# Performance work log

Measured on AMD Instinct MI355X. Metric: run time of the kernel, lower is better.

Reference implementation:

```python
import jax, jax.numpy as jnp
import numpy as np

B, N, DK = 16, 2048, 512

def setup_inputs() -> dict:
    key = jax.random.key(0)
    k1, k2, k3, k4 = jax.random.split(key, 4)
    return {
        'src_embedding': jax.random.normal(k1, (B, N, DK), dtype=jnp.float32),
        'target_embedding': jax.random.normal(k2, (B, N, DK), dtype=jnp.float32),
        'src': jax.random.normal(k3, (B, N, 3), dtype=jnp.float32),
        'target': jax.random.normal(k4, (B, N, 3), dtype=jnp.float32),
    }

def reference(src_embedding, target_embedding, src, target):
    d_k = src_embedding.shape[2]
    # attention-weighted soft correspondence: [B, N, M]
    scores = jnp.einsum('bnd,bmd->bnm', src_embedding, target_embedding)
    scores = jax.nn.softmax(scores / jnp.sqrt(jnp.asarray(d_k, scores.dtype)), axis=2)
    tgt_corr = jnp.einsum('bnm,bmc->bnc', scores, src)            # [B, N, 3]
    tgt_mean = jnp.mean(target, axis=1, keepdims=True)            # [B, 1, 3]
    corr_mean = jnp.mean(tgt_corr, axis=1, keepdims=True)         # [B, 1, 3]
    # cross-covariance H = (target - mu_t)^T @ (tgt_corr - mu_c): [B, 3, 3]
    H = jnp.einsum('bnc,bnd->bcd', target - tgt_mean, tgt_corr - corr_mean)
    U, S, Vh = jnp.linalg.svd(H)                                  # H = U diag(S) Vh
    det = jnp.linalg.det(jnp.matmul(U, Vh))                       # [B]
    # C = diag(1, 1, det) reflection fix; R = U @ C @ Vh
    diag = jnp.stack([jnp.ones_like(det), jnp.ones_like(det), det], axis=-1)  # [B, 3]
    R = jnp.matmul(U * diag[:, None, :], Vh)                      # [B, 3, 3]
    # t^T = mu_t^T - R @ mu_c^T, returned as [B, 1, 3]
    t = tgt_mean - jnp.einsum('bij,bkj->bki', R, corr_mean)
    return (R, t)
```

## Files before the change

kernel.cpp:

```cpp
#include <hip/hip_runtime.h>
#include <hip/hip_bf16.h>
#include <stdint.h>


#define B_  16
#define N_  2048
#define DK_ 512
#define SCALE 0.044194173824159216f

typedef __bf16 bf16x8 __attribute__((ext_vector_type(8)));
typedef float  f32x16 __attribute__((ext_vector_type(16)));
typedef float  f32x4  __attribute__((ext_vector_type(4)));

union BF8 { bf16x8 v; unsigned u[4]; };

__device__ inline unsigned pkbf(float a, float b) {
  unsigned r;
  asm("v_cvt_pk_bf16_f32 %0, %1, %2" : "=v"(r) : "v"(a), "v"(b));
  return r;
}

__global__ __launch_bounds__(512, 2)
void attn_stats_kernel(const float* __restrict__ Q, const float* __restrict__ K,
                       const float* __restrict__ Vsrc, float* __restrict__ part)
{
  __shared__ __align__(16) unsigned char s_k[32 * 1024];
  __shared__ __align__(16) float s_srcT[3 * 1024];

  const int L   = blockIdx.x;
  const int xcd = L & 7;
  const int kk  = L >> 3;
  const int b   = xcd + 8 * (kk & 1);
  const int ms  = (kk >> 1) & 1;
  const int nb  = kk >> 2;

  const int tid  = threadIdx.x;
  const int lane = tid & 63;
  const int wid  = tid >> 6;
  const int row  = lane & 31;
  const int hi   = lane >> 5;

  const int mchunk0 = ms * 1024;

  {
    const float* vp = Vsrc + ((size_t)b * N_ + mchunk0) * 3;
    for (int idx = tid; idx < 3072; idx += 512) {
      int m = idx / 3, c = idx - 3 * m;
      s_srcT[c * 1024 + m] = vp[idx];
    }
  }

  const int qglob = nb * 256 + wid * 32 + row;
  BF8 qf[32];
  {
    const f32x4* qp = (const f32x4*)(Q + ((size_t)b * N_ + qglob) * DK_);
    #pragma unroll
    for (int t = 0; t < 32; ++t) {
      f32x4 f0 = qp[t * 4 + hi * 2];
      f32x4 f1 = qp[t * 4 + hi * 2 + 1];
      qf[t].u[0] = pkbf(f0[0], f0[1]);
      qf[t].u[1] = pkbf(f0[2], f0[3]);
      qf[t].u[2] = pkbf(f1[0], f1[1]);
      qf[t].u[3] = pkbf(f1[2], f1[3]);
    }
  }

  const f32x4* kg = (const f32x4*)(K + ((size_t)b * N_ + mchunk0) * DK_);

  float lsum = 0.f, a0 = 0.f, a1 = 0.f, a2 = 0.f;

  f32x4 stg[8];
  #pragma unroll
  for (int i = 0; i < 8; ++i) stg[i] = kg[i * 512 + tid];

  const unsigned kread_base = (unsigned)(row * 1024);
  const unsigned kread_xor  = (unsigned)(row << 4);

  for (int tile = 0; tile < 32; ++tile) {
    __syncthreads();
    #pragma unroll
    for (int i = 0; i < 8; ++i) {
      int idx  = i * 512 + tid;
      int r    = idx >> 7;
      int colb = (idx & 127) * 8;
      unsigned addr = (unsigned)(r * 1024) + ((unsigned)colb ^ ((unsigned)(r << 4)));
      uint2 w2;
      w2.x = pkbf(stg[i][0], stg[i][1]);
      w2.y = pkbf(stg[i][2], stg[i][3]);
      *(uint2*)(s_k + addr) = w2;
    }
    __syncthreads();
    if (tile + 1 < 32) {
      const f32x4* kt = kg + (size_t)(tile + 1) * 4096;
      #pragma unroll
      for (int i = 0; i < 8; ++i) stg[i] = kt[i * 512 + tid];
    }
    f32x16 sc0, sc1;
    #pragma unroll
    for (int i = 0; i < 16; ++i) { sc0[i] = 0.f; sc1[i] = 0.f; }
    #pragma unroll
    for (int t = 0; t < 32; t += 2) {
      BF8 kf0, kf1;
      kf0.v = *(const bf16x8*)(s_k + kread_base +
                (((unsigned)(t * 32 + hi * 16)) ^ kread_xor));
      sc0 = __builtin_amdgcn_mfma_f32_32x32x16_bf16(kf0.v, qf[t].v, sc0, 0, 0, 0);
      kf1.v = *(const bf16x8*)(s_k + kread_base +
                (((unsigned)((t + 1) * 32 + hi * 16)) ^ kread_xor));
      sc1 = __builtin_amdgcn_mfma_f32_32x32x16_bf16(kf1.v, qf[t + 1].v, sc1, 0, 0, 0);
    }
    #pragma unroll
    for (int j = 0; j < 4; ++j) {
      const int mrun = tile * 32 + j * 8 + hi * 4;
      f32x4 s0 = *(const f32x4*)&s_srcT[mrun];
      f32x4 s1 = *(const f32x4*)&s_srcT[1024 + mrun];
      f32x4 s2 = *(const f32x4*)&s_srcT[2048 + mrun];
      #pragma unroll
      for (int i2 = 0; i2 < 4; ++i2) {
        float w = __expf((sc0[j * 4 + i2] + sc1[j * 4 + i2]) * SCALE);
        lsum += w;
        a0 += w * s0[i2];
        a1 += w * s1[i2];
        a2 += w * s2[i2];
      }
    }
  }

  a0   += __shfl_xor(a0, 32);
  a1   += __shfl_xor(a1, 32);
  a2   += __shfl_xor(a2, 32);
  lsum += __shfl_xor(lsum, 32);

  if (hi == 0) {
    f32x4 o; o[0] = a0; o[1] = a1; o[2] = a2; o[3] = lsum;
    *(f32x4*)(part + (((size_t)ms * B_ + b) * N_ + qglob) * 4) = o;
  }
}

__global__ void reduce_kernel(const float* __restrict__ part,
                              const float* __restrict__ tgt,
                              float* __restrict__ ws2)
{
  const int b = blockIdx.x, tid = threadIdx.x;
  float s[15];
  #pragma unroll
  for (int j = 0; j < 15; ++j) s[j] = 0.f;

  for (int n = tid; n < N_; n += 256) {
    f32x4 p0 = *(const f32x4*)(part + (((size_t)0 * B_ + b) * N_ + n) * 4);
    f32x4 p1 = *(const f32x4*)(part + (((size_t)1 * B_ + b) * N_ + n) * 4);
    float inv = 1.0f / (p0[3] + p1[3]);
    float c0 = (p0[0] + p1[0]) * inv;
    float c1 = (p0[1] + p1[1]) * inv;
    float c2 = (p0[2] + p1[2]) * inv;
    const float* tp = tgt + ((size_t)b * N_ + n) * 3;
    float t0 = tp[0], t1 = tp[1], t2 = tp[2];
    s[0] += t0;  s[1] += t1;  s[2] += t2;
    s[3] += c0;  s[4] += c1;  s[5] += c2;
    s[6] += t0 * c0;  s[7]  += t0 * c1;  s[8]  += t0 * c2;
    s[9] += t1 * c0;  s[10] += t1 * c1;  s[11] += t1 * c2;
    s[12] += t2 * c0; s[13] += t2 * c1;  s[14] += t2 * c2;
  }
  #pragma unroll
  for (int j = 0; j < 15; ++j) {
    #pragma unroll
    for (int off = 32; off > 0; off >>= 1) s[j] += __shfl_xor(s[j], off);
  }
  __shared__ float red[4][15];
  int lane = tid & 63, w = tid >> 6;
  if (lane == 0) {
    #pragma unroll
    for (int j = 0; j < 15; ++j) red[w][j] = s[j];
  }
  __syncthreads();
  if (tid < 15)
    ws2[b * 16 + tid] = red[0][tid] + red[1][tid] + red[2][tid] + red[3][tid];
}

__device__ inline void jrot(double A[3][3], double V[3][3], int p, int q) {
  double apq = A[p][q];
  if (fabs(apq) < 1e-300) return;
  double tau = (A[q][q] - A[p][p]) / (2.0 * apq);
  double tt = (tau >= 0.0) ? 1.0 / (tau + sqrt(1.0 + tau * tau))
                           : 1.0 / (tau - sqrt(1.0 + tau * tau));
  double c = 1.0 / sqrt(1.0 + tt * tt), sn = tt * c;
  for (int k = 0; k < 3; ++k) {
    double akp = A[k][p], akq = A[k][q];
    A[k][p] = c * akp - sn * akq;
    A[k][q] = sn * akp + c * akq;
  }
  for (int k = 0; k < 3; ++k) {
    double apk = A[p][k], aqk = A[q][k];
    A[p][k] = c * apk - sn * aqk;
    A[q][k] = sn * apk + c * aqk;
  }
  for (int k = 0; k < 3; ++k) {
    double vkp = V[k][p], vkq = V[k][q];
    V[k][p] = c * vkp - sn * vkq;
    V[k][q] = sn * vkp + c * vkq;
  }
}

__global__ void svd_kernel(const float* __restrict__ ws2, float* __restrict__ out)
{
  const int b = threadIdx.x;
  if (b >= B_) return;
  const float* s = ws2 + b * 16;
  const double invN = 1.0 / (double)N_;
  double stv[3] = {s[0], s[1], s[2]};
  double scv[3] = {s[3], s[4], s[5]};
  double H[3][3];
  for (int c = 0; c < 3; ++c)
    for (int d = 0; d < 3; ++d)
      H[c][d] = (double)s[6 + c * 3 + d] - stv[c] * scv[d] * invN;

  double A[3][3], V[3][3] = {{1,0,0},{0,1,0},{0,0,1}};
  for (int i = 0; i < 3; ++i)
    for (int j = 0; j < 3; ++j) {
      double acc = 0.0;
      for (int c = 0; c < 3; ++c) acc += H[c][i] * H[c][j];
      A[i][j] = acc;
    }
  for (int sw = 0; sw < 15; ++sw) { jrot(A,V,0,1); jrot(A,V,0,2); jrot(A,V,1,2); }

  double e[3] = {A[0][0], A[1][1], A[2][2]};
  double vc[3][3];
  for (int k = 0; k < 3; ++k)
    for (int i = 0; i < 3; ++i) vc[k][i] = V[i][k];
  for (int a2 = 0; a2 < 2; ++a2)
    for (int b2 = 0; b2 < 2 - a2; ++b2)
      if (e[b2] < e[b2 + 1]) {
        double te = e[b2]; e[b2] = e[b2 + 1]; e[b2 + 1] = te;
        for (int i = 0; i < 3; ++i) {
          double tv = vc[b2][i]; vc[b2][i] = vc[b2 + 1][i]; vc[b2 + 1][i] = tv;
        }
      }

  double u1[3], u2[3], u3[3];
  for (int i = 0; i < 3; ++i)
    u1[i] = H[i][0]*vc[0][0] + H[i][1]*vc[0][1] + H[i][2]*vc[0][2];
  double n1 = sqrt(u1[0]*u1[0] + u1[1]*u1[1] + u1[2]*u1[2]);
  n1 = fmax(n1, 1e-300);
  for (int i = 0; i < 3; ++i) u1[i] /= n1;
  for (int i = 0; i < 3; ++i)
    u2[i] = H[i][0]*vc[1][0] + H[i][1]*vc[1][1] + H[i][2]*vc[1][2];
  double d12 = u1[0]*u2[0] + u1[1]*u2[1] + u1[2]*u2[2];
  for (int i = 0; i < 3; ++i) u2[i] -= d12 * u1[i];
  double n2 = sqrt(u2[0]*u2[0] + u2[1]*u2[1] + u2[2]*u2[2]);
  n2 = fmax(n2, 1e-300);
  for (int i = 0; i < 3; ++i) u2[i] /= n2;
  u3[0] = u1[1]*u2[2] - u1[2]*u2[1];
  u3[1] = u1[2]*u2[0] - u1[0]*u2[2];
  u3[2] = u1[0]*u2[1] - u1[1]*u2[0];

  double detV = vc[0][0]*(vc[1][1]*vc[2][2] - vc[1][2]*vc[2][1])
              - vc[0][1]*(vc[1][0]*vc[2][2] - vc[1][2]*vc[2][0])
              + vc[0][2]*(vc[1][0]*vc[2][1] - vc[1][1]*vc[2][0]);

  double R[3][3];
  for (int i = 0; i < 3; ++i)
    for (int j = 0; j < 3; ++j)
      R[i][j] = u1[i]*vc[0][j] + u2[i]*vc[1][j] + detV * u3[i]*vc[2][j];

  for (int i = 0; i < 3; ++i)
    for (int j = 0; j < 3; ++j)
      out[b * 9 + i * 3 + j] = (float)R[i][j];

  double muc[3] = {scv[0]*invN, scv[1]*invN, scv[2]*invN};
  for (int i = 0; i < 3; ++i) {
    double ti = stv[i]*invN - (R[i][0]*muc[0] + R[i][1]*muc[1] + R[i][2]*muc[2]);
    out[B_ * 9 + b * 3 + i] = (float)ti;
  }
}

extern "C" void kernel_launch(void* const* d_in, const int* in_sizes, int n_in,
                              void* d_out, int out_size, void* d_ws, size_t ws_size,
                              hipStream_t stream)
{
  const float* srcE = (const float*)d_in[0];
  const float* tgtE = (const float*)d_in[1];
  const float* srcP = (const float*)d_in[2];
  const float* tgtP = (const float*)d_in[3];
  float* out  = (float*)d_out;
  float* part = (float*)d_ws;
  float* ws2  = part + (size_t)2 * B_ * N_ * 4;

  attn_stats_kernel<<<dim3(256), dim3(512), 0, stream>>>(srcE, tgtE, srcP, part);
  reduce_kernel<<<dim3(B_), dim3(256), 0, stream>>>(part, tgtP, ws2);
  svd_kernel<<<dim3(1), dim3(64), 0, stream>>>(ws2, out);
}
```

Measured before the change: 143.5 us.

## Double-buffer K tiles in LDS with smaller blocks and half-K stages

Measured after the change: 357.5 us. 2.49x slower.

```diff
diff --git a/kernel.cpp b/kernel.cpp
--- a/kernel.cpp
+++ b/kernel.cpp
@@ -20,19 +20,20 @@
   return r;
 }
 
-__global__ __launch_bounds__(512, 2)
+__global__ __launch_bounds__(256, 2)
 void attn_stats_kernel(const float* __restrict__ Q, const float* __restrict__ K,
                        const float* __restrict__ Vsrc, float* __restrict__ part)
 {
-  __shared__ __align__(16) unsigned char s_k[32 * 1024];
+  __shared__ __align__(16) unsigned char s_k[2][32 * 256 * 2];
   __shared__ __align__(16) float s_srcT[3 * 1024];
 
   const int L   = blockIdx.x;
   const int xcd = L & 7;
-  const int kk  = L >> 3;
-  const int b   = xcd + 8 * (kk & 1);
-  const int ms  = (kk >> 1) & 1;
-  const int nb  = kk >> 2;
+  const int k   = L >> 3;
+  const int b   = xcd + 8 * (k & 1);
+  const int rem = k >> 1;
+  const int nb  = rem & 15;
+  const int ms  = rem >> 4;
 
   const int tid  = threadIdx.x;
   const int lane = tid & 63;
@@ -44,13 +45,13 @@
 
   {
     const float* vp = Vsrc + ((size_t)b * N_ + mchunk0) * 3;
-    for (int idx = tid; idx < 3072; idx += 512) {
+    for (int idx = tid; idx < 3072; idx += 256) {
       int m = idx / 3, c = idx - 3 * m;
       s_srcT[c * 1024 + m] = vp[idx];
     }
   }
 
-  const int qglob = nb * 256 + wid * 32 + row;
+  const int qglob = nb * 128 + wid * 32 + row;
   BF8 qf[32];
   {
     const f32x4* qp = (const f32x4*)(Q + ((size_t)b * N_ + qglob) * DK_);
@@ -67,62 +68,90 @@
 
   const f32x4* kg = (const f32x4*)(K + ((size_t)b * N_ + mchunk0) * DK_);
 
+  #define STG_LOAD(u)                                                        \
+    {                                                                        \
+      const int mt_ = (u) >> 1, h_ = (u) & 1;                                \
+      _Pragma("unroll")                                                      \
+      for (int i = 0; i < 8; ++i) {                                          \
+        int idx = i * 256 + tid;                                             \
+        int r_  = idx >> 6, c4 = idx & 63;                                   \
+        stg[i] = kg[(size_t)(mt_ * 32 + r_) * 128 + h_ * 64 + c4];           \
+      }                                                                      \
+    }
+
+  #define STG_WRITE(bb)                                                      \
+    {                                                                        \
+      _Pragma("unroll")                                                      \
+      for (int i = 0; i < 8; ++i) {                                          \
+        int idx = i * 256 + tid;                                             \
+        int r_  = idx >> 6;                                                  \
+        unsigned colb = (unsigned)((idx & 63) * 8);                          \
+        unsigned addr = (unsigned)(r_ * 512) + (colb ^ ((unsigned)((r_ & 7) << 4))); \
+        uint2 w2;                                                            \
+        w2.x = pkbf(stg[i][0], stg[i][1]);                                   \
+        w2.y = pkbf(stg[i][2], stg[i][3]);                                   \
+        *(uint2*)(&s_k[bb][0] + addr) = w2;                                  \
+      }                                                                      \
+    }
+
+  f32x4 stg[8];
   float lsum = 0.f, a0 = 0.f, a1 = 0.f, a2 = 0.f;
 
-  f32x4 stg[8];
+  f32x16 sc0, sc1;
   #pragma unroll
-  for (int i = 0; i < 8; ++i) stg[i] = kg[i * 512 + tid];
-
-  const unsigned kread_base = (unsigned)(row * 1024);
-  const unsigned kread_xor  = (unsigned)(row << 4);
-
-  for (int tile = 0; tile < 32; ++tile) {
+  for (int i = 0; i < 16; ++i) { sc0[i] = 0.f; sc1[i] = 0.f; }
+
+  STG_LOAD(0)
+  STG_WRITE(0)
+  STG_LOAD(1)
+  __syncthreads();
+
+  const unsigned kread_base = (unsigned)(row * 512);
+  const unsigned kread_xor  = (unsigned)((row & 7) << 4);
+
+  const int NT = 64;
+  for (int t = 0; t < NT; ++t) {
+    const int cur = t & 1;
+    if (t + 1 < NT) STG_WRITE(cur ^ 1)
+    if (t + 2 < NT) STG_LOAD(t + 2)
+
+    const int h = t & 1;
+    const unsigned char* bp = &s_k[cur][0];
+    __builtin_amdgcn_s_setprio(1);
+    #pragma unroll
+    for (int ks = 0; ks < 16; ks += 2) {
+      BF8 kf0, kf1;
+      kf0.v = *(const bf16x8*)(bp + kread_base +
+                (((unsigned)(ks * 32 + hi * 16)) ^ kread_xor));
+      sc0 = __builtin_amdgcn_mfma_f32_32x32x16_bf16(kf0.v, qf[h * 16 + ks].v, sc0, 0, 0, 0);
+      kf1.v = *(const bf16x8*)(bp + kread_base +
+                (((unsigned)((ks + 1) * 32 + hi * 16)) ^ kread_xor));
+      sc1 = __builtin_amdgcn_mfma_f32_32x32x16_bf16(kf1.v, qf[h * 16 + ks + 1].v, sc1, 0, 0, 0);
+    }
+    __builtin_amdgcn_s_setprio(0);
+
+    if (t & 1) {
+      const int mt = t >> 1;
+      #pragma unroll
+      for (int j = 0; j < 4; ++j) {
+        const int mrun = mt * 32 + j * 8 + hi * 4;
+        f32x4 s0 = *(const f32x4*)&s_srcT[mrun];
+        f32x4 s1 = *(const f32x4*)&s_srcT[1024 + mrun];
+        f32x4 s2 = *(const f32x4*)&s_srcT[2048 + mrun];
+        #pragma unroll
+        for (int i2 = 0; i2 < 4; ++i2) {
+          float w = __expf((sc0[j * 4 + i2] + sc1[j * 4 + i2]) * SCALE);
+          lsum += w;
+          a0 += w * s0[i2];
+          a1 += w * s1[i2];
+          a2 += w * s2[i2];
+        }
+      }
+      #pragma unroll
+      for (int i = 0; i < 16; ++i) { sc0[i] = 0.f; sc1[i] = 0.f; }
+    }
+
     __syncthreads();
-    #pragma unroll
-    for (int i = 0; i < 8; ++i) {
-      int idx  = i * 512 + tid;
-      int r    = idx >> 7;
-      int colb = (idx & 127) * 8;
-      unsigned addr = (unsigned)(r * 1024) + ((unsigned)colb ^ ((unsigned)(r << 4)));
-      uint2 w2;
-      w2.x = pkbf(stg[i][0], stg[i][1]);
-      w2.y = pkbf(stg[i][2], stg[i][3]);
-      *(uint2*)(s_k + addr) = w2;
-    }
-    __syncthreads();
-    if (tile + 1 < 32) {
-      const f32x4* kt = kg + (size_t)(tile + 1) * 4096;
-      #pragma unroll
-      for (int i = 0; i < 8; ++i) stg[i] = kt[i * 512 + tid];
-    }
-    f32x16 sc0, sc1;
-    #pragma unroll
-    for (int i = 0; i < 16; ++i) { sc0[i] = 0.f; sc1[i] = 0.f; }
-    #pragma unroll
-    for (int t = 0; t < 32; t += 2) {
-      BF8 kf0, kf1;
-      kf0.v = *(const bf16x8*)(s_k + kread_base +
-                (((unsigned)(t * 32 + hi * 16)) ^ kread_xor));
-      sc0 = __builtin_amdgcn_mfma_f32_32x32x16_bf16(kf0.v, qf[t].v, sc0, 0, 0, 0);
-      kf1.v = *(const bf16x8*)(s_k + kread_base +
-                (((unsigned)((t + 1) * 32 + hi * 16)) ^ kread_xor));
-      sc1 = __builtin_amdgcn_mfma_f32_32x32x16_bf16(kf1.v, qf[t + 1].v, sc1, 0, 0, 0);
-    }
-    #pragma unroll
-    for (int j = 0; j < 4; ++j) {
-      const int mrun = tile * 32 + j * 8 + hi * 4;
-      f32x4 s0 = *(const f32x4*)&s_srcT[mrun];
-      f32x4 s1 = *(const f32x4*)&s_srcT[1024 + mrun];
-      f32x4 s2 = *(const f32x4*)&s_srcT[2048 + mrun];
-      #pragma unroll
-      for (int i2 = 0; i2 < 4; ++i2) {
-        float w = __expf((sc0[j * 4 + i2] + sc1[j * 4 + i2]) * SCALE);
-        lsum += w;
-        a0 += w * s0[i2];
-        a1 += w * s1[i2];
-        a2 += w * s2[i2];
-      }
-    }
   }
 
   a0   += __shfl_xor(a0, 32);
@@ -134,6 +163,8 @@
     f32x4 o; o[0] = a0; o[1] = a1; o[2] = a2; o[3] = lsum;
     *(f32x4*)(part + (((size_t)ms * B_ + b) * N_ + qglob) * 4) = o;
   }
+  #undef STG_LOAD
+  #undef STG_WRITE
 }
 
 __global__ void reduce_kernel(const float* __restrict__ part,
@@ -284,7 +315,7 @@
   float* part = (float*)d_ws;
   float* ws2  = part + (size_t)2 * B_ * N_ * 4;
 
-  attn_stats_kernel<<<dim3(256), dim3(512), 0, stream>>>(srcE, tgtE, srcP, part);
+  attn_stats_kernel<<<dim3(512), dim3(256), 0, stream>>>(srcE, tgtE, srcP, part);
   reduce_kernel<<<dim3(B_), dim3(256), 0, stream>>>(part, tgtP, ws2);
   svd_kernel<<<dim3(1), dim3(64), 0, stream>>>(ws2, out);
 }
```

## Remap attention blocks so each processes two batches over strided key windows

Applied to the files above, without the earlier changes.

Result: slower. 175.5 us (+22.3%).

```diff
diff --git a/kernel.cpp b/kernel.cpp
--- a/kernel.cpp
+++ b/kernel.cpp
@@ -25,14 +25,13 @@
                        const float* __restrict__ Vsrc, float* __restrict__ part)
 {
   __shared__ __align__(16) unsigned char s_k[32 * 1024];
-  __shared__ __align__(16) float s_srcT[3 * 1024];
+  __shared__ __align__(16) float s_srcT[3 * 256];
 
   const int L   = blockIdx.x;
-  const int xcd = L & 7;
-  const int kk  = L >> 3;
-  const int b   = xcd + 8 * (kk & 1);
-  const int ms  = (kk >> 1) & 1;
-  const int nb  = kk >> 2;
+  const int x   = L & 7;
+  const int cu  = L >> 3;
+  const int nb  = cu & 7;
+  const int sms = cu >> 3;
 
   const int tid  = threadIdx.x;
   const int lane = tid & 63;
@@ -40,99 +39,110 @@
   const int row  = lane & 31;
   const int hi   = lane >> 5;
 
-  const int mchunk0 = ms * 1024;
-
-  {
-    const float* vp = Vsrc + ((size_t)b * N_ + mchunk0) * 3;
-    for (int idx = tid; idx < 3072; idx += 512) {
-      int m = idx / 3, c = idx - 3 * m;
-      s_srcT[c * 1024 + m] = vp[idx];
-    }
-  }
-
   const int qglob = nb * 256 + wid * 32 + row;
-  BF8 qf[32];
-  {
-    const f32x4* qp = (const f32x4*)(Q + ((size_t)b * N_ + qglob) * DK_);
-    #pragma unroll
-    for (int t = 0; t < 32; ++t) {
-      f32x4 f0 = qp[t * 4 + hi * 2];
-      f32x4 f1 = qp[t * 4 + hi * 2 + 1];
-      qf[t].u[0] = pkbf(f0[0], f0[1]);
-      qf[t].u[1] = pkbf(f0[2], f0[3]);
-      qf[t].u[2] = pkbf(f1[0], f1[1]);
-      qf[t].u[3] = pkbf(f1[2], f1[3]);
-    }
-  }
-
-  const f32x4* kg = (const f32x4*)(K + ((size_t)b * N_ + mchunk0) * DK_);
-
-  float lsum = 0.f, a0 = 0.f, a1 = 0.f, a2 = 0.f;
-
-  f32x4 stg[8];
-  #pragma unroll
-  for (int i = 0; i < 8; ++i) stg[i] = kg[i * 512 + tid];
 
   const unsigned kread_base = (unsigned)(row * 1024);
   const unsigned kread_xor  = (unsigned)(row << 4);
 
-  for (int tile = 0; tile < 32; ++tile) {
-    __syncthreads();
-    #pragma unroll
-    for (int i = 0; i < 8; ++i) {
-      int idx  = i * 512 + tid;
-      int r    = idx >> 7;
-      int colb = (idx & 127) * 8;
-      unsigned addr = (unsigned)(r * 1024) + ((unsigned)colb ^ ((unsigned)(r << 4)));
-      uint2 w2;
-      w2.x = pkbf(stg[i][0], stg[i][1]);
-      w2.y = pkbf(stg[i][2], stg[i][3]);
-      *(uint2*)(s_k + addr) = w2;
-    }
-    __syncthreads();
-    if (tile + 1 < 32) {
-      const f32x4* kt = kg + (size_t)(tile + 1) * 4096;
+  BF8   qf[32];
+  f32x4 stg[8];
+
+  for (int half = 0; half < 2; ++half) {
+    const int b = x + 8 * half;
+
+    {
+      const f32x4* qp = (const f32x4*)(Q + ((size_t)b * N_ + qglob) * DK_);
       #pragma unroll
-      for (int i = 0; i < 8; ++i) stg[i] = kt[i * 512 + tid];
-    }
-    f32x16 sc0, sc1;
-    #pragma unroll
-    for (int i = 0; i < 16; ++i) { sc0[i] = 0.f; sc1[i] = 0.f; }
-    #pragma unroll
-    for (int t = 0; t < 32; t += 2) {
-      BF8 kf0, kf1;
-      kf0.v = *(const bf16x8*)(s_k + kread_base +
-                (((unsigned)(t * 32 + hi * 16)) ^ kread_xor));
-      sc0 = __builtin_amdgcn_mfma_f32_32x32x16_bf16(kf0.v, qf[t].v, sc0, 0, 0, 0);
-      kf1.v = *(const bf16x8*)(s_k + kread_base +
-                (((unsigned)((t + 1) * 32 + hi * 16)) ^ kread_xor));
-      sc1 = __builtin_amdgcn_mfma_f32_32x32x16_bf16(kf1.v, qf[t + 1].v, sc1, 0, 0, 0);
-    }
-    #pragma unroll
-    for (int j = 0; j < 4; ++j) {
-      const int mrun = tile * 32 + j * 8 + hi * 4;
-      f32x4 s0 = *(const f32x4*)&s_srcT[mrun];
-      f32x4 s1 = *(const f32x4*)&s_srcT[1024 + mrun];
-      f32x4 s2 = *(const f32x4*)&s_srcT[2048 + mrun];
-      #pragma unroll
-      for (int i2 = 0; i2 < 4; ++i2) {
-        float w = __expf((sc0[j * 4 + i2] + sc1[j * 4 + i2]) * SCALE);
-        lsum += w;
-        a0 += w * s0[i2];
-        a1 += w * s1[i2];
-        a2 += w * s2[i2];
+      for (int t = 0; t < 32; ++t) {
+        f32x4 f0 = qp[t * 4 + hi * 2];
+        f32x4 f1 = qp[t * 4 + hi * 2 + 1];
+        qf[t].u[0] = pkbf(f0[0], f0[1]);
+        qf[t].u[1] = pkbf(f0[2], f0[3]);
+        qf[t].u[2] = pkbf(f1[0], f1[1]);
+        qf[t].u[3] = pkbf(f1[2], f1[3]);
       }
     }
-  }
-
-  a0   += __shfl_xor(a0, 32);
-  a1   += __shfl_xor(a1, 32);
-  a2   += __shfl_xor(a2, 32);
-  lsum += __shfl_xor(lsum, 32);
-
-  if (hi == 0) {
-    f32x4 o; o[0] = a0; o[1] = a1; o[2] = a2; o[3] = lsum;
-    *(f32x4*)(part + (((size_t)ms * B_ + b) * N_ + qglob) * 4) = o;
+
+    float lsum = 0.f, a0 = 0.f, a1 = 0.f, a2 = 0.f;
+
+    for (int ph = 0; ph < 2; ++ph) {
+      const int mwin = ph * 1024 + sms * 256;
+      const f32x4* kg = (const f32x4*)(K + ((size_t)b * N_ + mwin) * DK_);
+
+      __syncthreads();
+
+      {
+        const float* vp = Vsrc + ((size_t)b * N_ + mwin) * 3;
+        for (int idx = tid; idx < 768; idx += 512) {
+          int m = idx / 3, c = idx - 3 * m;
+          s_srcT[c * 256 + m] = vp[idx];
+        }
+      }
+
+      #pragma unroll
+      for (int i = 0; i < 8; ++i) stg[i] = kg[i * 512 + tid];
+
+      for (int t = 0; t < 8; ++t) {
+        __syncthreads();
+        #pragma unroll
+        for (int i = 0; i < 8; ++i) {
+          int idx  = i * 512 + tid;
+          int r    = idx >> 7;
+          int colb = (idx & 127) * 8;
+          unsigned addr = (unsigned)(r * 1024) + ((unsigned)colb ^ ((unsigned)(r << 4)));
+          uint2 w2;
+          w2.x = pkbf(stg[i][0], stg[i][1]);
+          w2.y = pkbf(stg[i][2], stg[i][3]);
+          *(uint2*)(s_k + addr) = w2;
+        }
+        __syncthreads();
+        if (t + 1 < 8) {
+          const f32x4* kt = kg + (size_t)(t + 1) * 4096;
+          #pragma unroll
+          for (int i = 0; i < 8; ++i) stg[i] = kt[i * 512 + tid];
+        }
+        f32x16 sc0, sc1;
+        #pragma unroll
+        for (int i = 0; i < 16; ++i) { sc0[i] = 0.f; sc1[i] = 0.f; }
+        __builtin_amdgcn_s_setprio(1);
+        #pragma unroll
+        for (int ks = 0; ks < 32; ks += 2) {
+          BF8 kf0, kf1;
+          kf0.v = *(const bf16x8*)(s_k + kread_base +
+                    (((unsigned)(ks * 32 + hi * 16)) ^ kread_xor));
+          sc0 = __builtin_amdgcn_mfma_f32_32x32x16_bf16(kf0.v, qf[ks].v, sc0, 0, 0, 0);
+          kf1.v = *(const bf16x8*)(s_k + kread_base +
+                    (((unsigned)((ks + 1) * 32 + hi * 16)) ^ kread_xor));
+          sc1 = __builtin_amdgcn_mfma_f32_32x32x16_bf16(kf1.v, qf[ks + 1].v, sc1, 0, 0, 0);
+        }
+        __builtin_amdgcn_s_setprio(0);
+        #pragma unroll
+        for (int j = 0; j < 4; ++j) {
+          const int mrun = t * 32 + j * 8 + hi * 4;
+          f32x4 s0 = *(const f32x4*)&s_srcT[mrun];
+          f32x4 s1 = *(const f32x4*)&s_srcT[256 + mrun];
+          f32x4 s2 = *(const f32x4*)&s_srcT[512 + mrun];
+          #pragma unroll
+          for (int i2 = 0; i2 < 4; ++i2) {
+            float w = __expf((sc0[j * 4 + i2] + sc1[j * 4 + i2]) * SCALE);
+            lsum += w;
+            a0 += w * s0[i2];
+            a1 += w * s1[i2];
+            a2 += w * s2[i2];
+          }
+        }
+      }
+    }
+
+    a0   += __shfl_xor(a0, 32);
+    a1   += __shfl_xor(a1, 32);
+    a2   += __shfl_xor(a2, 32);
+    lsum += __shfl_xor(lsum, 32);
+
+    if (hi == 0) {
+      f32x4 o; o[0] = a0; o[1] = a1; o[2] = a2; o[3] = lsum;
+      *(f32x4*)(part + (((size_t)sms * B_ + b) * N_ + qglob) * 4) = o;
+    }
   }
 }
 
@@ -148,10 +158,13 @@
   for (int n = tid; n < N_; n += 256) {
     f32x4 p0 = *(const f32x4*)(part + (((size_t)0 * B_ + b) * N_ + n) * 4);
     f32x4 p1 = *(const f32x4*)(part + (((size_t)1 * B_ + b) * N_ + n) * 4);
-    float inv = 1.0f / (p0[3] + p1[3]);
-    float c0 = (p0[0] + p1[0]) * inv;
-    float c1 = (p0[1] + p1[1]) * inv;
-    float c2 = (p0[2] + p1[2]) * inv;
+    f32x4 p2 = *(const f32x4*)(part + (((size_t)2 * B_ + b) * N_ + n) * 4);
+    f32x4 p3 = *(const f32x4*)(part + (((size_t)3 * B_ + b) * N_ + n) * 4);
+    float l  = p0[3] + p1[3] + p2[3] + p3[3];
+    float inv = 1.0f / l;
+    float c0 = (p0[0] + p1[0] + p2[0] + p3[0]) * inv;
+    float c1 = (p0[1] + p1[1] + p2[1] + p3[1]) * inv;
+    float c2 = (p0[2] + p1[2] + p2[2] + p3[2]) * inv;
     const float* tp = tgt + ((size_t)b * N_ + n) * 3;
     float t0 = tp[0], t1 = tp[1], t2 = tp[2];
     s[0] += t0;  s[1] += t1;  s[2] += t2;
@@ -282,7 +295,7 @@
   const float* tgtP = (const float*)d_in[3];
   float* out  = (float*)d_out;
   float* part = (float*)d_ws;
-  float* ws2  = part + (size_t)2 * B_ * N_ * 4;
+  float* ws2  = part + (size_t)4 * B_ * N_ * 4;
 
   attn_stats_kernel<<<dim3(256), dim3(512), 0, stream>>>(srcE, tgtE, srcP, part);
   reduce_kernel<<<dim3(B_), dim3(256), 0, stream>>>(part, tgtP, ws2);
```

## Pre-convert K to bf16 and stream tiles into double-buffered LDS via direct loads

Applied to the files above, without the earlier changes.

New measurement: 131.8 us. 1.09x faster.

```diff
diff --git a/kernel.cpp b/kernel.cpp
--- a/kernel.cpp
+++ b/kernel.cpp
@@ -20,9 +20,149 @@
   return r;
 }
 
+__device__ inline void gl_lds16(const void* g, void* l) {
+  __builtin_amdgcn_global_load_lds(
+      (const __attribute__((address_space(1))) unsigned int*)g,
+      (__attribute__((address_space(3))) unsigned int*)l, 16, 0, 0);
+}
+
+__global__ __launch_bounds__(256)
+void cvt_k_kernel(const float* __restrict__ in, uint4* __restrict__ out)
+{
+  const size_t total = (size_t)B_ * N_ * DK_ / 8;
+  for (size_t i = (size_t)blockIdx.x * 256 + threadIdx.x; i < total;
+       i += (size_t)gridDim.x * 256) {
+    f32x4 a = ((const f32x4*)in)[2 * i];
+    f32x4 c = ((const f32x4*)in)[2 * i + 1];
+    uint4 w;
+    w.x = pkbf(a[0], a[1]);
+    w.y = pkbf(a[2], a[3]);
+    w.z = pkbf(c[0], c[1]);
+    w.w = pkbf(c[2], c[3]);
+    out[i] = w;
+  }
+}
+
 __global__ __launch_bounds__(512, 2)
-void attn_stats_kernel(const float* __restrict__ Q, const float* __restrict__ K,
+void attn_stats_kernel(const float* __restrict__ Q,
+                       const unsigned char* __restrict__ Kbf,
                        const float* __restrict__ Vsrc, float* __restrict__ part)
+{
+  __shared__ __align__(16) unsigned char s_k[2][32 * 1024];
+  __shared__ __align__(16) float s_srcT[3 * 1024];
+
+  const int L   = blockIdx.x;
+  const int xcd = L & 7;
+  const int kk  = L >> 3;
+  const int b   = xcd + 8 * (kk & 1);
+  const int ms  = (kk >> 1) & 1;
+  const int nb  = kk >> 2;
+
+  const int tid  = threadIdx.x;
+  const int lane = tid & 63;
+  const int wid  = tid >> 6;
+  const int row  = lane & 31;
+  const int hi   = lane >> 5;
+
+  const int mchunk0 = ms * 1024;
+
+  {
+    const float* vp = Vsrc + ((size_t)b * N_ + mchunk0) * 3;
+    for (int idx = tid; idx < 3072; idx += 512) {
+      int m = idx / 3, c = idx - 3 * m;
+      s_srcT[c * 1024 + m] = vp[idx];
+    }
+  }
+
+  const int qglob = nb * 256 + wid * 32 + row;
+  BF8 qf[32];
+  {
+    const f32x4* qp = (const f32x4*)(Q + ((size_t)b * N_ + qglob) * DK_);
+    #pragma unroll
+    for (int t = 0; t < 32; ++t) {
+      f32x4 f0 = qp[t * 4 + hi * 2];
+      f32x4 f1 = qp[t * 4 + hi * 2 + 1];
+      qf[t].u[0] = pkbf(f0[0], f0[1]);
+      qf[t].u[1] = pkbf(f0[2], f0[3]);
+      qf[t].u[2] = pkbf(f1[0], f1[1]);
+      qf[t].u[3] = pkbf(f1[2], f1[3]);
+    }
+  }
+
+  const unsigned char* kbase = Kbf + ((size_t)b * N_ + mchunk0) * (DK_ * 2);
+
+  #define STAGE(bb, t)                                                       \
+    { _Pragma("unroll")                                                      \
+      for (int j = 0; j < 4; ++j) {                                          \
+        const int r_ = wid * 4 + j;                                          \
+        gl_lds16(kbase + (((size_t)(t) * 32 + r_) << 10)                     \
+                       + (unsigned)((lane ^ r_) << 4),                       \
+                 &s_k[bb][r_ << 10]);                                        \
+      } }
+
+  float lsum = 0.f, a0 = 0.f, a1 = 0.f, a2 = 0.f;
+
+  const unsigned kread_base = (unsigned)(row * 1024);
+  const unsigned kread_xor  = (unsigned)(row << 4);
+
+  STAGE(0, 0)
+  __syncthreads();
+
+  for (int tile = 0; tile < 32; ++tile) {
+    const int cur = tile & 1;
+    if (tile + 1 < 32) STAGE(cur ^ 1, tile + 1)
+
+    const unsigned char* bp = &s_k[cur][0];
+    f32x16 sc0, sc1;
+    #pragma unroll
+    for (int i = 0; i < 16; ++i) { sc0[i] = 0.f; sc1[i] = 0.f; }
+    __builtin_amdgcn_s_setprio(1);
+    #pragma unroll
+    for (int t = 0; t < 32; t += 2) {
+      BF8 kf0, kf1;
+      kf0.v = *(const bf16x8*)(bp + kread_base +
+                (((unsigned)(t * 32 + hi * 16)) ^ kread_xor));
+      sc0 = __builtin_amdgcn_mfma_f32_32x32x16_bf16(kf0.v, qf[t].v, sc0, 0, 0, 0);
+      kf1.v = *(const bf16x8*)(bp + kread_base +
+                (((unsigned)((t + 1) * 32 + hi * 16)) ^ kread_xor));
+      sc1 = __builtin_amdgcn_mfma_f32_32x32x16_bf16(kf1.v, qf[t + 1].v, sc1, 0, 0, 0);
+    }
+    __builtin_amdgcn_s_setprio(0);
+
+    #pragma unroll
+    for (int j = 0; j < 4; ++j) {
+      const int mrun = tile * 32 + j * 8 + hi * 4;
+      f32x4 s0 = *(const f32x4*)&s_srcT[mrun];
+      f32x4 s1 = *(const f32x4*)&s_srcT[1024 + mrun];
+      f32x4 s2 = *(const f32x4*)&s_srcT[2048 + mrun];
+      #pragma unroll
+      for (int i2 = 0; i2 < 4; ++i2) {
+        float w = __expf((sc0[j * 4 + i2] + sc1[j * 4 + i2]) * SCALE);
+        lsum += w;
+        a0 += w * s0[i2];
+        a1 += w * s1[i2];
+        a2 += w * s2[i2];
+      }
+    }
+
+    __syncthreads();
+  }
+  #undef STAGE
+
+  a0   += __shfl_xor(a0, 32);
+  a1   += __shfl_xor(a1, 32);
+  a2   += __shfl_xor(a2, 32);
+  lsum += __shfl_xor(lsum, 32);
+
+  if (hi == 0) {
+    f32x4 o; o[0] = a0; o[1] = a1; o[2] = a2; o[3] = lsum;
+    *(f32x4*)(part + (((size_t)ms * B_ + b) * N_ + qglob) * 4) = o;
+  }
+}
+
+__global__ __launch_bounds__(512, 2)
+void attn_stats_f32_kernel(const float* __restrict__ Q, const float* __restrict__ K,
+                           const float* __restrict__ Vsrc, float* __restrict__ part)
 {
   __shared__ __align__(16) unsigned char s_k[32 * 1024];
   __shared__ __align__(16) float s_srcT[3 * 1024];
@@ -98,6 +238,7 @@
     f32x16 sc0, sc1;
     #pragma unroll
     for (int i = 0; i < 16; ++i) { sc0[i] = 0.f; sc1[i] = 0.f; }
+    __builtin_amdgcn_s_setprio(1);
     #pragma unroll
     for (int t = 0; t < 32; t += 2) {
       BF8 kf0, kf1;
@@ -108,6 +249,7 @@
                 (((unsigned)((t + 1) * 32 + hi * 16)) ^ kread_xor));
       sc1 = __builtin_amdgcn_mfma_f32_32x32x16_bf16(kf1.v, qf[t + 1].v, sc1, 0, 0, 0);
     }
+    __builtin_amdgcn_s_setprio(0);
     #pragma unroll
     for (int j = 0; j < 4; ++j) {
       const int mrun = tile * 32 + j * 8 + hi * 4;
@@ -280,11 +422,24 @@
   const float* tgtE = (const float*)d_in[1];
   const float* srcP = (const float*)d_in[2];
   const float* tgtP = (const float*)d_in[3];
-  float* out  = (float*)d_out;
-  float* part = (float*)d_ws;
-  float* ws2  = part + (size_t)2 * B_ * N_ * 4;
-
-  attn_stats_kernel<<<dim3(256), dim3(512), 0, stream>>>(srcE, tgtE, srcP, part);
-  reduce_kernel<<<dim3(B_), dim3(256), 0, stream>>>(part, tgtP, ws2);
-  svd_kernel<<<dim3(1), dim3(64), 0, stream>>>(ws2, out);
-}
+  float* out = (float*)d_out;
+
+  const size_t kbf_bytes   = (size_t)B_ * N_ * DK_ * 2;
+  const size_t part_floats = (size_t)2 * B_ * N_ * 4;
+
+  if (ws_size >= kbf_bytes + part_floats * 4 + 1024) {
+    unsigned char* kbf = (unsigned char*)d_ws;
+    float* part = (float*)(kbf + kbf_bytes);
+    float* ws2  = part + part_floats;
+    cvt_k_kernel<<<dim3(2048), dim3(256), 0, stream>>>(tgtE, (uint4*)kbf);
+    attn_stats_kernel<<<dim3(256), dim3(512), 0, stream>>>(srcE, kbf, srcP, part);
+    reduce_kernel<<<dim3(B_), dim3(256), 0, stream>>>(part, tgtP, ws2);
+    svd_kernel<<<dim3(1), dim3(64), 0, stream>>>(ws2, out);
+  } else {
+    float* part = (float*)d_ws;
+    float* ws2  = part + part_floats;
+    attn_stats_f32_kernel<<<dim3(256), dim3(512), 0, stream>>>(srcE, tgtE, srcP, part);
+    reduce_kernel<<<dim3(B_), dim3(256), 0, stream>>>(part, tgtP, ws2);
+    svd_kernel<<<dim3(1), dim3(64), 0, stream>>>(ws2, out);
+  }
+}
```
